# Optimization experiments

Hardware: AMD Instinct MI355X
Metric: run time of the kernel (lower is better)

## Reference

```python
import jax, jax.numpy as jnp
import numpy as np

T, B, D, H = 512, 64, 1024, 1024  # seq_len, batch, input_dim, hidden_dim


def setup_inputs() -> dict:
    key = jax.random.key(0)
    k1, k2, k3, k4 = jax.random.split(key, 4)
    x = jax.random.normal(k1, (T, B, D), dtype=jnp.float32)
    # nn.Linear default init scale ~ 1/sqrt(fan_in)
    s = 1.0 / np.sqrt(D + H)
    Wfc = jax.random.normal(k2, (2 * H, D + H), dtype=jnp.float32) * s   # fc weight
    Wfc2 = jax.random.normal(k3, (H, D + H), dtype=jnp.float32) * s     # fc2 weight
    # xavier_normal_ for w_hh: std = sqrt(2/(fan_in+fan_out)) = sqrt(2/(D+H+1))
    w_hh = jax.random.normal(k4, (1, D + H), dtype=jnp.float32) * np.sqrt(2.0 / (D + H + 1))
    bias = jnp.zeros((), dtype=jnp.float32)  # reset_weigths sets bias to scalar 0.0
    return {"x": x, "Wfc": Wfc, "Wfc2": Wfc2, "w_hh": w_hh, "bias": bias}


def reference(x, Wfc, Wfc2, w_hh, bias):
    # GRU-style ConvLSTMCell driven over the time loop (num_layers=1).
    Tn, Bn, Dn = x.shape
    Hn = Wfc2.shape[0]
    h0 = jnp.full((Bn, Hn), 1e-9, dtype=x.dtype)  # init_hidden: zeros + 1e-9

    def step(h, xt):
        combined = jnp.concatenate([xt, h], axis=1)          # [B, D+H]
        cc = combined @ Wfc.T                                 # [B, 2H]
        z = jax.nn.sigmoid(cc[:, :Hn])
        r = jax.nn.sigmoid(cc[:, Hn:])
        combined2 = jnp.concatenate([xt, r * h], axis=1)      # [B, D+H]
        con2 = jnp.tanh(combined2 @ Wfc2.T)                   # [B, H]
        h_next = (1.0 - z) * h + z * con2
        delta_u = jax.nn.sigmoid(combined @ w_hh.T + bias) / 100.0  # [B, 1]
        return h_next, (h_next, delta_u)

    _, (h_seq, _delta_u_seq) = jax.lax.scan(step, h0, x)
    return h_seq  # [T, B, H]
```

## Files before the change

### kernel.cpp

```cpp
#include <hip/hip_runtime.h>
#include <hip/hip_bf16.h>
#include <stdint.h>


typedef float  f32x4  __attribute__((ext_vector_type(4)));
typedef int    i32x4  __attribute__((ext_vector_type(4)));
typedef __bf16 bf16x8 __attribute__((ext_vector_type(8)));

#define NWG 64
#define TSTEPS 512

#define XALL_OFF 0UL
#define XALL_BYTES (32768UL * 3072UL * 2UL)
#define WXP_OFF   (XALL_OFF + XALL_BYTES)
#define WXP_BYTES (3072UL * 1024UL * 2UL)
#define HBUF_OFF  (WXP_OFF + WXP_BYTES)
#define RHBUF_OFF (HBUF_OFF + 262144UL)
#define FLAG_OFF  (RHBUF_OFF + 262144UL)
#define WS_NEED   (FLAG_OFF + 8192UL)

#define GL_LDS16(g, l) __builtin_amdgcn_global_load_lds( \
    (const __attribute__((address_space(1))) void*)(const void*)(g), \
    (__attribute__((address_space(3))) void*)(void*)(l), 16, 0, 0)

#define ASM_LD16(dst, p) \
  asm volatile("global_load_dwordx4 %0, %1, off sc0 sc1" \
               : "=&v"(dst) : "v"(p) : "memory")
#define ASM_ST16(p, v) \
  asm volatile("global_store_dwordx4 %0, %1, off sc0 sc1" \
               :: "v"(p), "v"(v) : "memory")
#define WAITV(N) do { asm volatile("s_waitcnt vmcnt(" #N ")" ::: "memory"); \
                      __builtin_amdgcn_sched_barrier(0); } while (0)

__device__ __forceinline__ unsigned short f2bf(float f) {
  __hip_bfloat16 h = __float2bfloat16(f);
  return __builtin_bit_cast(unsigned short, h);
}
__device__ __forceinline__ bf16x8 ld16(const void* p) {
  return __builtin_bit_cast(bf16x8, *(const uint4*)p);
}
__device__ __forceinline__ i32x4 ldi4(const void* p) {
  return __builtin_bit_cast(i32x4, *(const uint4*)p);
}
__device__ __forceinline__ f32x4 mfma16(bf16x8 a, bf16x8 b, f32x4 c) {
  return __builtin_amdgcn_mfma_f32_16x16x32_bf16(a, b, c, 0, 0, 0);
}
__device__ __forceinline__ float sigm(float x) {
  return __builtin_amdgcn_rcpf(1.0f + __builtin_amdgcn_exp2f(-1.4426950408889634f * x));
}
__device__ __forceinline__ float tanh_fast(float x) {
  return 1.0f - 2.0f * __builtin_amdgcn_rcpf(1.0f + __builtin_amdgcn_exp2f(2.8853900817779268f * x));
}

__global__ void cvt_x(const float* __restrict__ x, __hip_bfloat16* __restrict__ o) {
  size_t i = ((size_t)blockIdx.x * 256 + threadIdx.x) * 4;
  float4 v = *(const float4*)(x + i);
  ushort4 u; u.x = f2bf(v.x); u.y = f2bf(v.y); u.z = f2bf(v.z); u.w = f2bf(v.w);
  *(ushort4*)(o + i) = u;
}

__global__ void pack_w(const float* __restrict__ Wfc, const float* __restrict__ Wfc2,
                       __hip_bfloat16* __restrict__ Wxp) {
  int row = blockIdx.x;
  int k = threadIdx.x * 4;
  const float* src = (row < 2048) ? (Wfc + (size_t)row * 2048 + k)
                                  : (Wfc2 + (size_t)(row - 2048) * 2048 + k);
  float4 v = *(const float4*)src;
  ushort4 u; u.x = f2bf(v.x); u.y = f2bf(v.y); u.z = f2bf(v.z); u.w = f2bf(v.w);
  *(ushort4*)(Wxp + (size_t)row * 1024 + k) = u;
}

__global__ void init_k(__hip_bfloat16* __restrict__ hbuf,
                       int* __restrict__ flagh, int* __restrict__ flagr) {
  size_t i = ((size_t)blockIdx.x * 256 + threadIdx.x) * 4;
  unsigned short hv = f2bf(1e-9f);
  ushort4 u; u.x = hv; u.y = hv; u.z = hv; u.w = hv;
  *(ushort4*)(hbuf + i) = u;
  if (blockIdx.x == 0 && threadIdx.x < 64)
    __hip_atomic_store(&flagh[threadIdx.x << 4], 1, __ATOMIC_RELAXED, __HIP_MEMORY_SCOPE_AGENT);
  if (blockIdx.x == 1 && threadIdx.x < 64)
    __hip_atomic_store(&flagr[threadIdx.x << 4], 0, __ATOMIC_RELAXED, __HIP_MEMORY_SCOPE_AGENT);
}

__global__ void __launch_bounds__(256) gemm_xw(const __hip_bfloat16* __restrict__ A,
                                               const __hip_bfloat16* __restrict__ B,
                                               __hip_bfloat16* __restrict__ C) {
  __shared__ __hip_bfloat16 As[128 * 64];
  __shared__ __hip_bfloat16 Bs[128 * 64];
  const int tid = threadIdx.x, lane = tid & 63, wv = tid >> 6;
  const int bn = blockIdx.x, bm = blockIdx.y;
  const int wm = wv >> 1, wn = wv & 1;
  const int n = lane & 15, q = lane >> 4;
  f32x4 acc[4][4];
#pragma unroll
  for (int i = 0; i < 4; ++i)
#pragma unroll
    for (int j = 0; j < 4; ++j) acc[i][j] = (f32x4){0.f, 0.f, 0.f, 0.f};
  const __hip_bfloat16* Ab = A + (size_t)bm * 128 * 1024;
  const __hip_bfloat16* Bb = B + (size_t)bn * 128 * 1024;
  for (int ko = 0; ko < 1024; ko += 64) {
#pragma unroll
    for (int r = 0; r < 4; ++r) {
      int chunk = r * 256 + wv * 64 + lane;
      int row = chunk >> 3, c16 = chunk & 7;
      GL_LDS16(Ab + (size_t)row * 1024 + ko + c16 * 8, (char*)As + (r * 256 + wv * 64) * 16);
      GL_LDS16(Bb + (size_t)row * 1024 + ko + c16 * 8, (char*)Bs + (r * 256 + wv * 64) * 16);
    }
    __syncthreads();
#pragma unroll
    for (int ks = 0; ks < 2; ++ks) {
      bf16x8 af[4], bfr[4];
#pragma unroll
      for (int mi = 0; mi < 4; ++mi)
        af[mi] = ld16((const char*)As + (wm * 64 + mi * 16 + n) * 128 + ks * 64 + q * 16);
#pragma unroll
      for (int ni = 0; ni < 4; ++ni)
        bfr[ni] = ld16((const char*)Bs + (wn * 64 + ni * 16 + n) * 128 + ks * 64 + q * 16);
#pragma unroll
      for (int mi = 0; mi < 4; ++mi)
#pragma unroll
        for (int ni = 0; ni < 4; ++ni)
          acc[mi][ni] = mfma16(af[mi], bfr[ni], acc[mi][ni]);
    }
    __syncthreads();
  }
#pragma unroll
  for (int mi = 0; mi < 4; ++mi)
#pragma unroll
    for (int ni = 0; ni < 4; ++ni) {
      int col = bn * 128 + wn * 64 + ni * 16 + n;
#pragma unroll
      for (int r = 0; r < 4; ++r) {
        int row = bm * 128 + wm * 64 + mi * 16 + q * 4 + r;
        C[(size_t)row * 3072 + col] = __float2bfloat16(acc[mi][ni][r]);
      }
    }
}

__device__ __forceinline__ void wait_flags(const int* flags, int target, int wv, int lane) {
  if (wv == 0) {
    const int* fp = flags + (lane << 4);
    while (!__all(__hip_atomic_load(fp, __ATOMIC_RELAXED, __HIP_MEMORY_SCOPE_AGENT) >= target))
      __builtin_amdgcn_s_sleep(1);
  }
  __syncthreads();
}
__device__ __forceinline__ void publish(int* p, int v) {
  asm volatile("s_waitcnt vmcnt(0)" ::: "memory");
  __syncthreads();
  if (threadIdx.x == 0)
    asm volatile("global_store_dword %0, %1, off sc0 sc1" :: "v"(p), "v"(v) : "memory");
}

__global__ void __launch_bounds__(256, 1) rec_k(
    const float* __restrict__ Wfc, const float* __restrict__ Wfc2,
    const __hip_bfloat16* __restrict__ xall,
    __hip_bfloat16* __restrict__ hbuf,
    __hip_bfloat16* __restrict__ rhbuf,
    float* __restrict__ out,
    int* __restrict__ flagh, int* __restrict__ flagr) {
  __shared__ __hip_bfloat16 W1s[32 * 1024];
  __shared__ __hip_bfloat16 W2s[16 * 1024];
  __shared__ char Pks[4 * 512];
  const int g = blockIdx.x, tid = threadIdx.x;
  const int lane = tid & 63, wv = tid >> 6;
  const int n = lane & 15, q = lane >> 4;
  const int gc = g * 16;

  {
    const int k0 = tid * 4;
    for (int j = 0; j < 32; ++j) {
      int grow = (j < 16) ? (gc + j) : (1024 + gc + (j - 16));
      float4 v = *(const float4*)(Wfc + (size_t)grow * 2048 + 1024 + k0);
      ushort4 u; u.x = f2bf(v.x); u.y = f2bf(v.y); u.z = f2bf(v.z); u.w = f2bf(v.w);
      *(ushort4*)((char*)W1s + j * 2048 + ((k0 * 2) ^ ((j & 7) << 4))) = u;
    }
    for (int j = 0; j < 16; ++j) {
      float4 v = *(const float4*)(Wfc2 + (size_t)(gc + j) * 2048 + 1024 + k0);
      ushort4 u; u.x = f2bf(v.x); u.y = f2bf(v.y); u.z = f2bf(v.z); u.w = f2bf(v.w);
      *(ushort4*)((char*)W2s + j * 2048 + ((k0 * 2) ^ ((j & 7) << 4))) = u;
    }
  }
  __syncthreads();

  const int m0 = wv * 16 + q * 4;
  const int arow = wv * 16 + n;
  const int col = gc + n;
  const char* w1z = (const char*)W1s + n * 2048;
  const char* w1r = (const char*)W1s + (16 + n) * 2048;
  const char* w2b = (const char*)W2s + n * 2048;
  const int sw = (n & 7) << 4;
  const int goff = q * 1024 + arow * 16;
  char* pk = Pks + wv * 512;
  const int wr_off = (n >> 3) * 256 + (n & 7) * 2;
  const int hi = lane >> 4 & 1;
  const int r16 = lane & 15;
  const int st_off = (2 * g + hi) * 1024 + (wv * 16 + r16) * 16;

  float hf[4] = {1e-9f, 1e-9f, 1e-9f, 1e-9f};
  float xz[4], xrr[4], xc[4];
  {
    const __hip_bfloat16* xr = xall;
#pragma unroll
    for (int r = 0; r < 4; ++r) {
      xz[r]  = __bfloat162float(xr[(m0 + r) * 3072 + col]);
      xrr[r] = __bfloat162float(xr[(m0 + r) * 3072 + 1024 + col]);
      xc[r]  = __bfloat162float(xr[(m0 + r) * 3072 + 2048 + col]);
    }
  }

  for (int t = 0; t < TSTEPS; ++t) {
    wait_flags(flagh, t + 1, wv, lane);
    const char* hApt = (const char*)hbuf + (t & 1) * 131072 + goff;
    bf16x8 ha[32];
#pragma unroll
    for (int ks = 0; ks < 32; ++ks) ASM_LD16(ha[ks], hApt + ks * 4096);
    f32x4 az = (f32x4){0.f, 0.f, 0.f, 0.f}, ar = (f32x4){0.f, 0.f, 0.f, 0.f};
    WAITV(16);
#pragma unroll
    for (int ks = 0; ks < 16; ++ks) {
      az = mfma16(ha[ks], ld16(w1z + ((ks * 64 + q * 16) ^ sw)), az);
      ar = mfma16(ha[ks], ld16(w1r + ((ks * 64 + q * 16) ^ sw)), ar);
    }
    WAITV(0);
#pragma unroll
    for (int ks = 16; ks < 32; ++ks) {
      az = mfma16(ha[ks], ld16(w1z + ((ks * 64 + q * 16) ^ sw)), az);
      ar = mfma16(ha[ks], ld16(w1r + ((ks * 64 + q * 16) ^ sw)), ar);
    }
    float z4[4];
#pragma unroll
    for (int r = 0; r < 4; ++r) {
      z4[r] = sigm(az[r] + xz[r]);
      float rrh = sigm(ar[r] + xrr[r]) * hf[r];
      *(unsigned short*)(pk + wr_off + (q * 4 + r) * 16) = f2bf(rrh);
    }
    __syncthreads();
    if (lane < 32) {
      i32x4 w = ldi4(pk + (lane >> 4) * 256 + r16 * 16);
      char* dst = (char*)rhbuf + (t & 1) * 131072 + st_off;
      ASM_ST16(dst, w);
    }
    publish(flagr + g * 16, t + 1);

    wait_flags(flagr, t + 1, wv, lane);
    const char* rApt = (const char*)rhbuf + (t & 1) * 131072 + goff;
#pragma unroll
    for (int ks = 0; ks < 32; ++ks) ASM_LD16(ha[ks], rApt + ks * 4096);
    f32x4 ac = (f32x4){0.f, 0.f, 0.f, 0.f};
    WAITV(16);
#pragma unroll
    for (int ks = 0; ks < 16; ++ks)
      ac = mfma16(ha[ks], ld16(w2b + ((ks * 64 + q * 16) ^ sw)), ac);
    WAITV(0);
#pragma unroll
    for (int ks = 16; ks < 32; ++ks)
      ac = mfma16(ha[ks], ld16(w2b + ((ks * 64 + q * 16) ^ sw)), ac);
#pragma unroll
    for (int r = 0; r < 4; ++r) {
      float th = tanh_fast(ac[r] + xc[r]);
      float hn = hf[r] + z4[r] * (th - hf[r]);
      hf[r] = hn;
      *(unsigned short*)(pk + wr_off + (q * 4 + r) * 16) = f2bf(hn);
    }
    __syncthreads();
    if (lane < 32) {
      i32x4 w = ldi4(pk + (lane >> 4) * 256 + r16 * 16);
      char* dst = (char*)hbuf + ((t + 1) & 1) * 131072 + st_off;
      ASM_ST16(dst, w);
    }
    publish(flagh + g * 16, t + 2);

#pragma unroll
    for (int r = 0; r < 4; ++r)
      out[((size_t)t * 64 + m0 + r) * 1024 + col] = hf[r];
    const int tn = (t + 1 < TSTEPS) ? t + 1 : t;
    const __hip_bfloat16* xr = xall + (size_t)tn * 64 * 3072;
#pragma unroll
    for (int r = 0; r < 4; ++r) {
      xz[r]  = __bfloat162float(xr[(m0 + r) * 3072 + col]);
      xrr[r] = __bfloat162float(xr[(m0 + r) * 3072 + 1024 + col]);
      xc[r]  = __bfloat162float(xr[(m0 + r) * 3072 + 2048 + col]);
    }
  }
}

extern "C" void kernel_launch(void* const* d_in, const int* in_sizes, int n_in,
                              void* d_out, int out_size, void* d_ws, size_t ws_size,
                              hipStream_t stream) {
  if (ws_size < WS_NEED) return;
  const float* x    = (const float*)d_in[0];
  const float* Wfc  = (const float*)d_in[1];
  const float* Wfc2 = (const float*)d_in[2];
  float* out = (float*)d_out;
  char* ws = (char*)d_ws;

  __hip_bfloat16* xall  = (__hip_bfloat16*)(ws + XALL_OFF);
  __hip_bfloat16* Wxp   = (__hip_bfloat16*)(ws + WXP_OFF);
  __hip_bfloat16* hbuf  = (__hip_bfloat16*)(ws + HBUF_OFF);
  __hip_bfloat16* rhbuf = (__hip_bfloat16*)(ws + RHBUF_OFF);
  int* flagh            = (int*)(ws + FLAG_OFF);
  int* flagr            = (int*)(ws + FLAG_OFF + 4096);
  __hip_bfloat16* Xbf   = (__hip_bfloat16*)d_out;

  cvt_x<<<32768, 256, 0, stream>>>(x, Xbf);
  pack_w<<<3072, 256, 0, stream>>>(Wfc, Wfc2, Wxp);
  init_k<<<64, 256, 0, stream>>>(hbuf, flagh, flagr);
  gemm_xw<<<dim3(24, 256), 256, 0, stream>>>(Xbf, Wxp, xall);

  void* args[] = {(void*)&Wfc, (void*)&Wfc2, (void*)&xall, (void*)&hbuf,
                  (void*)&rhbuf, (void*)&out, (void*)&flagh, (void*)&flagr};
  (void)hipLaunchCooperativeKernel((void*)rec_k, dim3(NWG), dim3(256), args, 0, stream);
}
```

Baseline: 3.941 ms.

## Replace block-wide barriers with per-wave flags in recurrent kernel

Each wave now publishes its own progress flag (four slots per workgroup) and polls all 256 flags itself with a vector load, instead of one wave polling and then __syncthreads plus a thread-0 publish. The LDS pack exchange inside a wave uses a local lgkmcnt wait rather than a full block barrier. The aim is to remove the two block barriers per half-step from the latency-bound recurrence. In exchange every wave issues its own polling loads, which adds memory traffic, and the correctness of the LDS handoff now rests on it being wave-local.

Result: slower. 4.834 ms (+22.7%).

```diff
diff --git a/kernel.cpp b/kernel.cpp
--- a/kernel.cpp
+++ b/kernel.cpp
@@ -23,14 +23,19 @@
     (const __attribute__((address_space(1))) void*)(const void*)(g), \
     (__attribute__((address_space(3))) void*)(void*)(l), 16, 0, 0)
 
-#define ASM_LD16(dst, p) \
+#define LD16F(dst, p) \
   asm volatile("global_load_dwordx4 %0, %1, off sc0 sc1" \
                : "=&v"(dst) : "v"(p) : "memory")
-#define ASM_ST16(p, v) \
+#define ST16F(p, v) \
   asm volatile("global_store_dwordx4 %0, %1, off sc0 sc1" \
+               :: "v"(p), "v"(v) : "memory")
+#define ST4F(p, v) \
+  asm volatile("global_store_dword %0, %1, off sc0 sc1" \
                :: "v"(p), "v"(v) : "memory")
 #define WAITV(N) do { asm volatile("s_waitcnt vmcnt(" #N ")" ::: "memory"); \
                       __builtin_amdgcn_sched_barrier(0); } while (0)
+#define WAITLGKM() do { asm volatile("s_waitcnt lgkmcnt(0)" ::: "memory"); \
+                        __builtin_amdgcn_sched_barrier(0); } while (0)
 
 __device__ __forceinline__ unsigned short f2bf(float f) {
   __hip_bfloat16 h = __float2bfloat16(f);
@@ -76,10 +81,14 @@
   unsigned short hv = f2bf(1e-9f);
   ushort4 u; u.x = hv; u.y = hv; u.z = hv; u.w = hv;
   *(ushort4*)(hbuf + i) = u;
-  if (blockIdx.x == 0 && threadIdx.x < 64)
-    __hip_atomic_store(&flagh[threadIdx.x << 4], 1, __ATOMIC_RELAXED, __HIP_MEMORY_SCOPE_AGENT);
-  if (blockIdx.x == 1 && threadIdx.x < 64)
-    __hip_atomic_store(&flagr[threadIdx.x << 4], 0, __ATOMIC_RELAXED, __HIP_MEMORY_SCOPE_AGENT);
+  if (blockIdx.x == 0 && threadIdx.x < 256) {
+    int g = threadIdx.x >> 2, wv = threadIdx.x & 3;
+    __hip_atomic_store(&flagh[g * 16 + wv], 1, __ATOMIC_RELAXED, __HIP_MEMORY_SCOPE_AGENT);
+  }
+  if (blockIdx.x == 1 && threadIdx.x < 256) {
+    int g = threadIdx.x >> 2, wv = threadIdx.x & 3;
+    __hip_atomic_store(&flagr[g * 16 + wv], 0, __ATOMIC_RELAXED, __HIP_MEMORY_SCOPE_AGENT);
+  }
 }
 
 __global__ void __launch_bounds__(256) gemm_xw(const __hip_bfloat16* __restrict__ A,
@@ -137,19 +146,15 @@
     }
 }
 
-__device__ __forceinline__ void wait_flags(const int* flags, int target, int wv, int lane) {
-  if (wv == 0) {
-    const int* fp = flags + (lane << 4);
-    while (!__all(__hip_atomic_load(fp, __ATOMIC_RELAXED, __HIP_MEMORY_SCOPE_AGENT) >= target))
-      __builtin_amdgcn_s_sleep(1);
-  }
-  __syncthreads();
-}
-__device__ __forceinline__ void publish(int* p, int v) {
-  asm volatile("s_waitcnt vmcnt(0)" ::: "memory");
-  __syncthreads();
-  if (threadIdx.x == 0)
-    asm volatile("global_store_dword %0, %1, off sc0 sc1" :: "v"(p), "v"(v) : "memory");
+__device__ __forceinline__ void wait_flags_w(const char* fl, int target, int lane) {
+  for (;;) {
+    i32x4 f;
+    LD16F(f, fl + lane * 64);
+    WAITV(0);
+    int ok = (f[0] >= target) & (f[1] >= target) & (f[2] >= target) & (f[3] >= target);
+    if (__all(ok)) return;
+    __builtin_amdgcn_s_sleep(1);
+  }
 }
 
 __global__ void __launch_bounds__(256, 1) rec_k(
@@ -193,9 +198,11 @@
   const int goff = q * 1024 + arow * 16;
   char* pk = Pks + wv * 512;
   const int wr_off = (n >> 3) * 256 + (n & 7) * 2;
-  const int hi = lane >> 4 & 1;
+  const int hi = (lane >> 4) & 1;
   const int r16 = lane & 15;
   const int st_off = (2 * g + hi) * 1024 + (wv * 16 + r16) * 16;
+  const char* flh = (const char*)flagh;
+  const char* flr = (const char*)flagr;
 
   float hf[4] = {1e-9f, 1e-9f, 1e-9f, 1e-9f};
   float xz[4], xrr[4], xc[4];
@@ -210,11 +217,11 @@
   }
 
   for (int t = 0; t < TSTEPS; ++t) {
-    wait_flags(flagh, t + 1, wv, lane);
+    wait_flags_w(flh, t + 1, lane);
     const char* hApt = (const char*)hbuf + (t & 1) * 131072 + goff;
     bf16x8 ha[32];
 #pragma unroll
-    for (int ks = 0; ks < 32; ++ks) ASM_LD16(ha[ks], hApt + ks * 4096);
+    for (int ks = 0; ks < 32; ++ks) LD16F(ha[ks], hApt + ks * 4096);
     f32x4 az = (f32x4){0.f, 0.f, 0.f, 0.f}, ar = (f32x4){0.f, 0.f, 0.f, 0.f};
     WAITV(16);
 #pragma unroll
@@ -235,18 +242,18 @@
       float rrh = sigm(ar[r] + xrr[r]) * hf[r];
       *(unsigned short*)(pk + wr_off + (q * 4 + r) * 16) = f2bf(rrh);
     }
-    __syncthreads();
+    WAITLGKM();
     if (lane < 32) {
-      i32x4 w = ldi4(pk + (lane >> 4) * 256 + r16 * 16);
-      char* dst = (char*)rhbuf + (t & 1) * 131072 + st_off;
-      ASM_ST16(dst, w);
-    }
-    publish(flagr + g * 16, t + 1);
-
-    wait_flags(flagr, t + 1, wv, lane);
+      i32x4 w = ldi4(pk + hi * 256 + r16 * 16);
+      ST16F((char*)rhbuf + (t & 1) * 131072 + st_off, w);
+    }
+    WAITV(0);
+    if (lane == 0) ST4F(flr + g * 64 + wv * 4, t + 1);
+
+    wait_flags_w(flr, t + 1, lane);
     const char* rApt = (const char*)rhbuf + (t & 1) * 131072 + goff;
 #pragma unroll
-    for (int ks = 0; ks < 32; ++ks) ASM_LD16(ha[ks], rApt + ks * 4096);
+    for (int ks = 0; ks < 32; ++ks) LD16F(ha[ks], rApt + ks * 4096);
     f32x4 ac = (f32x4){0.f, 0.f, 0.f, 0.f};
     WAITV(16);
 #pragma unroll
@@ -263,13 +270,13 @@
       hf[r] = hn;
       *(unsigned short*)(pk + wr_off + (q * 4 + r) * 16) = f2bf(hn);
     }
-    __syncthreads();
+    WAITLGKM();
     if (lane < 32) {
-      i32x4 w = ldi4(pk + (lane >> 4) * 256 + r16 * 16);
-      char* dst = (char*)hbuf + ((t + 1) & 1) * 131072 + st_off;
-      ASM_ST16(dst, w);
-    }
-    publish(flagh + g * 16, t + 2);
+      i32x4 w = ldi4(pk + hi * 256 + r16 * 16);
+      ST16F((char*)hbuf + ((t + 1) & 1) * 131072 + st_off, w);
+    }
+    WAITV(0);
+    if (lane == 0) ST4F(flh + g * 64 + wv * 4, t + 2);
 
 #pragma unroll
     for (int r = 0; r < 4; ++r)
```
